# Optimization experiments

Measured on AMD Instinct MI355X. Metric: run time of the kernel, lower is better.

The kernel has to match this reference:

```python
import jax, jax.numpy as jnp
import numpy as np

B, L, D = 2, 2048, 4096
H, HKV = 32, 8
HD = D // H  # 128


def apply_rope(xq, xk, cos, sin):
    # xq: [B,L,H,HD], xk: [B,L,HKV,HD]; cos/sin: [L, HD//2]
    def rot(t):
        t2 = t.reshape(*t.shape[:-1], -1, 2)  # [..., HD//2, 2]
        tr, ti = t2[..., 0], t2[..., 1]
        c = cos[None, :, None, :]
        s = sin[None, :, None, :]
        out_r = tr * c - ti * s
        out_i = tr * s + ti * c
        return jnp.stack([out_r, out_i], axis=-1).reshape(t.shape)
    return rot(xq), rot(xk)


def setup_inputs() -> dict:
    key = jax.random.key(0)
    ks = jax.random.split(key, 5)
    sc = 0.02
    x = jax.random.normal(ks[0], (B, L, D), jnp.float32)
    wq = jax.random.normal(ks[1], (D, D), jnp.float32) * sc
    wk = jax.random.normal(ks[2], (HKV * HD, D), jnp.float32) * sc
    wv = jax.random.normal(ks[3], (HKV * HD, D), jnp.float32) * sc
    wo = jax.random.normal(ks[4], (D, D), jnp.float32) * sc
    # Llama RoPE tables
    inv_freq = 1.0 / (10000.0 ** (jnp.arange(0, HD, 2, dtype=jnp.float32) / HD))
    t = jnp.arange(L, dtype=jnp.float32)
    freqs = jnp.outer(t, inv_freq)  # [L, HD//2]
    cos, sin = jnp.cos(freqs), jnp.sin(freqs)
    # causal additive mask
    neg = jnp.float32(-1e9)
    mask = jnp.where(jnp.tril(jnp.ones((L, L), bool)), 0.0, neg)[None, None]
    return {"x": x, "wq": wq, "wk": wk, "wv": wv, "wo": wo,
            "cos": cos, "sin": sin, "mask": mask}


def reference(x, wq, wk, wv, wo, cos, sin, mask):
    Bx, Lx = x.shape[:2]
    xq = (x @ wq.T).reshape(Bx, Lx, H, HD)
    xk = (x @ wk.T).reshape(Bx, Lx, HKV, HD)
    xv = (x @ wv.T).reshape(Bx, Lx, HKV, HD)
    xq, xk = apply_rope(xq, xk, cos, sin)
    times = H // HKV
    xk = jnp.repeat(xk, times, axis=2)  # [B,L,H,HD]
    xv = jnp.repeat(xv, times, axis=2)
    # [B,H,L,L]
    scores = jnp.einsum('blhd,bmhd->bhlm', xq, xk) / jnp.sqrt(jnp.float32(HD))
    scores = scores + mask
    probs = jax.nn.softmax(scores.astype(jnp.float32), axis=-1).astype(xq.dtype)
    out = jnp.einsum('bhlm,bmhd->blhd', probs, xv).reshape(Bx, Lx, -1)
    return out @ wo.T
```

## Files before the change

kernel.cpp:

```cpp
#include <hip/hip_runtime.h>

#define BB 2
#define LL 2048
#define DD 4096
#define HH 32
#define NKV 8
#define HDIM 128
#define MROWS (BB*LL)

typedef __attribute__((ext_vector_type(8))) short bf16x8;
typedef __attribute__((ext_vector_type(8))) unsigned short u16x8;
typedef __attribute__((ext_vector_type(4))) unsigned short u16x4;
typedef __attribute__((ext_vector_type(4))) float f32x4;

#define MFMA16(a, b, c) __builtin_amdgcn_mfma_f32_16x16x32_bf16(a, b, c, 0, 0, 0)

__device__ __forceinline__ unsigned short f2bf(float x) {
  union { float f; unsigned u; } v; v.f = x;
  unsigned r = v.u + 0x7FFF + ((v.u >> 16) & 1);
  return (unsigned short)(r >> 16);
}
__device__ __forceinline__ float bf2f(unsigned short h) {
  union { unsigned u; float f; } v; v.u = ((unsigned)h) << 16; return v.f;
}
__device__ __forceinline__ unsigned packbf2(float lo, float hi) {
  return ((unsigned)f2bf(hi) << 16) | (unsigned)f2bf(lo);
}
__device__ __forceinline__ void gload_lds16(const void* g, void* l) {
  __builtin_amdgcn_global_load_lds(
      (const __attribute__((address_space(1))) unsigned int*)g,
      (__attribute__((address_space(3))) unsigned int*)l, 16, 0, 0);
}

__global__ __launch_bounds__(256) void cast_f32_bf16(
    const float* __restrict__ in, unsigned short* __restrict__ out, int n) {
  int stride = gridDim.x * blockDim.x * 4;
  for (int i = (blockIdx.x * blockDim.x + threadIdx.x) * 4; i < n; i += stride) {
    float4 v = *(const float4*)&in[i];
    u16x4 u;
    u[0] = f2bf(v.x); u[1] = f2bf(v.y); u[2] = f2bf(v.z); u[3] = f2bf(v.w);
    *(u16x4*)&out[i] = u;
  }
}

template <bool OUTBF>
__global__ __launch_bounds__(256) void gemm_bt(
    const unsigned short* __restrict__ A, const float* __restrict__ B,
    void* __restrict__ Cv, int M, int N, int K) {
  __shared__ unsigned short As[128 * 64];
  __shared__ unsigned short Bs[128 * 64];
  const int tid = threadIdx.x;
  const int lane = tid & 63, w = tid >> 6;
  const int l15 = lane & 15, lg = lane >> 4;
  const int wr = w >> 1, wc = w & 1;
  const int brow = blockIdx.y * 128, bcol = blockIdx.x * 128;

  f32x4 acc[4][4];
#pragma unroll
  for (int m = 0; m < 4; ++m)
#pragma unroll
    for (int n = 0; n < 4; ++n)
#pragma unroll
      for (int j = 0; j < 4; ++j) acc[m][n][j] = 0.f;

  for (int k0 = 0; k0 < K; k0 += 64) {
#pragma unroll
    for (int i = 0; i < 4; ++i) {
      int idx = i * 256 + tid;
      int row = idx >> 3, s = idx & 7;
      gload_lds16(&A[(size_t)(brow + row) * K + k0 + ((s ^ (row & 7)) * 8)],
                  &As[idx * 8]);
    }
#pragma unroll
    for (int i = 0; i < 4; ++i) {
      int f = i * 256 + tid;
      int row = f >> 3, s = f & 7;
      const float* src = &B[(size_t)(bcol + row) * K + k0 + ((s ^ (row & 7)) * 8)];
      float4 f0 = *(const float4*)src;
      float4 f1 = *(const float4*)(src + 4);
      u16x8 u;
      u[0] = f2bf(f0.x); u[1] = f2bf(f0.y); u[2] = f2bf(f0.z); u[3] = f2bf(f0.w);
      u[4] = f2bf(f1.x); u[5] = f2bf(f1.y); u[6] = f2bf(f1.z); u[7] = f2bf(f1.w);
      *(u16x8*)&Bs[f * 8] = u;
    }
    __syncthreads();
#pragma unroll
    for (int kk = 0; kk < 2; ++kk) {
      bf16x8 af[4], bfr[4];
      const int phys = (kk * 4 + lg) ^ (l15 & 7);
#pragma unroll
      for (int m = 0; m < 4; ++m) {
        int row = wr * 64 + m * 16 + l15;
        af[m] = *(const bf16x8*)&As[row * 64 + phys * 8];
      }
#pragma unroll
      for (int n = 0; n < 4; ++n) {
        int row = wc * 64 + n * 16 + l15;
        bfr[n] = *(const bf16x8*)&Bs[row * 64 + phys * 8];
      }
#pragma unroll
      for (int m = 0; m < 4; ++m)
#pragma unroll
        for (int n = 0; n < 4; ++n)
          acc[m][n] = MFMA16(af[m], bfr[n], acc[m][n]);
    }
    __syncthreads();
  }

#pragma unroll
  for (int m = 0; m < 4; ++m)
#pragma unroll
    for (int n = 0; n < 4; ++n)
#pragma unroll
      for (int j = 0; j < 4; ++j) {
        int r = brow + wr * 64 + m * 16 + lg * 4 + j;
        int c = bcol + wc * 64 + n * 16 + l15;
        if (OUTBF)
          ((unsigned short*)Cv)[(size_t)r * N + c] = f2bf(acc[m][n][j]);
        else
          ((float*)Cv)[(size_t)r * N + c] = acc[m][n][j];
      }
}

__global__ __launch_bounds__(256) void rope_bf16(
    unsigned* __restrict__ q, unsigned* __restrict__ k,
    const float* __restrict__ cosp, const float* __restrict__ sinp) {
  const int NQ = MROWS * (DD / 2);
  const int NT = NQ + MROWS * (NKV * HDIM / 2);
  int stride = gridDim.x * blockDim.x;
  for (int p = blockIdx.x * blockDim.x + threadIdx.x; p < NT; p += stride) {
    bool isq = p < NQ;
    int pp = isq ? p : p - NQ;
    int row = isq ? (pp >> 11) : (pp >> 9);
    int hp  = isq ? (pp & 2047) : (pp & 511);
    int i = hp & 63, l = row & (LL - 1);
    float c = cosp[l * 64 + i], s = sinp[l * 64 + i];
    unsigned* ptr = isq ? (q + (size_t)row * 2048 + hp)
                        : (k + (size_t)row * 512 + hp);
    unsigned v = *ptr;
    float tr = bf2f((unsigned short)(v & 0xffff));
    float ti = bf2f((unsigned short)(v >> 16));
    *ptr = packbf2(tr * c - ti * s, tr * s + ti * c);
  }
}

__global__ __launch_bounds__(256) void attn_mfma(
    const unsigned short* __restrict__ Qb, const unsigned short* __restrict__ Kb,
    const unsigned short* __restrict__ Vb, unsigned short* __restrict__ Ob) {
  __shared__ unsigned short Ks[64 * 128];
  __shared__ unsigned short Vt[128 * 64];
  const int tid = threadIdx.x;
  const int lane = tid & 63, w = tid >> 6;
  const int l15 = lane & 15, lg = lane >> 4;
  const int qt = (int)gridDim.x - 1 - (int)blockIdx.x;
  const int bh = blockIdx.y;
  const int b = bh >> 5, h = bh & 31, kvh = h >> 2;
  const int qrel = w * 16 + l15;
  const size_t qrow = (size_t)(b * LL + qt * 64 + qrel);

  bf16x8 qf[4];
#pragma unroll
  for (int c = 0; c < 4; ++c)
    qf[c] = *(const bf16x8*)&Qb[qrow * DD + h * HDIM + c * 32 + lg * 8];

  f32x4 oacc[8];
#pragma unroll
  for (int d = 0; d < 8; ++d)
#pragma unroll
    for (int j = 0; j < 4; ++j) oacc[d][j] = 0.f;
  float mrun = -1e30f, lrun = 0.f;
  const float scale = 0.08838834764831845f;

  for (int t0 = 0; t0 <= qt; ++t0) {
    const int k0 = t0 * 64;
#pragma unroll
    for (int i = 0; i < 4; ++i) {
      int idx = i * 256 + tid;
      int krow = idx >> 4, slot = idx & 15;
      gload_lds16(&Kb[(size_t)(b * LL + k0 + krow) * (NKV * HDIM) + kvh * HDIM +
                      ((slot ^ (krow & 15)) * 8)],
                  &Ks[idx * 8]);
    }
#pragma unroll
    for (int i = 0; i < 4; ++i) {
      int f = i * 256 + tid;
      int key = f & 63, d0 = (f >> 6) * 8;
      u16x8 v = *(const u16x8*)&Vb[(size_t)(b * LL + k0 + key) * (NKV * HDIM) +
                                   kvh * HDIM + d0];
#pragma unroll
      for (int j = 0; j < 8; ++j) {
        int dim = d0 + j;
        Vt[dim * 64 + (((key >> 3) ^ (dim & 7)) * 8) + (key & 7)] = v[j];
      }
    }
    __syncthreads();

    f32x4 sa[4];
#pragma unroll
    for (int mb = 0; mb < 4; ++mb) {
#pragma unroll
      for (int j = 0; j < 4; ++j) sa[mb][j] = 0.f;
#pragma unroll
      for (int c = 0; c < 4; ++c) {
        int row = mb * 16 + l15;
        int phys = (c * 4 + lg) ^ l15;
        bf16x8 kf = *(const bf16x8*)&Ks[row * 128 + phys * 8];
        sa[mb] = MFMA16(kf, qf[c], sa[mb]);
      }
    }

    const bool boundary = (t0 == qt);
#pragma unroll
    for (int mb = 0; mb < 4; ++mb)
#pragma unroll
      for (int j = 0; j < 4; ++j) {
        float s = sa[mb][j] * scale;
        if (boundary && (mb * 16 + lg * 4 + j > qrel)) s = -1e30f;
        sa[mb][j] = s;
      }
    float vm = -1e30f;
#pragma unroll
    for (int mb = 0; mb < 4; ++mb)
#pragma unroll
      for (int j = 0; j < 4; ++j) vm = fmaxf(vm, sa[mb][j]);
    vm = fmaxf(vm, __shfl_xor(vm, 16));
    vm = fmaxf(vm, __shfl_xor(vm, 32));
    float mnew = fmaxf(mrun, vm);
    float corr = __expf(mrun - mnew);
    float psum = 0.f;
#pragma unroll
    for (int mb = 0; mb < 4; ++mb)
#pragma unroll
      for (int j = 0; j < 4; ++j) {
        float p = __expf(sa[mb][j] - mnew);
        sa[mb][j] = p;
        psum += p;
      }
    psum += __shfl_xor(psum, 16);
    psum += __shfl_xor(psum, 32);
    lrun = lrun * corr + psum;
    mrun = mnew;
#pragma unroll
    for (int d = 0; d < 8; ++d)
#pragma unroll
      for (int j = 0; j < 4; ++j) oacc[d][j] *= corr;

    unsigned pk[4][2];
#pragma unroll
    for (int mb = 0; mb < 4; ++mb) {
      pk[mb][0] = packbf2(sa[mb][0], sa[mb][1]);
      pk[mb][1] = packbf2(sa[mb][2], sa[mb][3]);
    }

#pragma unroll
    for (int kh = 0; kh < 2; ++kh) {
      unsigned pbu[4];
#pragma unroll
      for (int r = 0; r < 4; ++r) {
        int srcl = l15 + 16 * ((lg & 1) * 2 + (r >> 1));
        unsigned va = (unsigned)__shfl((int)pk[2 * kh][r & 1], srcl);
        unsigned vb = (unsigned)__shfl((int)pk[2 * kh + 1][r & 1], srcl);
        pbu[r] = (lane & 32) ? vb : va;
      }
      bf16x8 pb;
#pragma unroll
      for (int r = 0; r < 4; ++r) {
        pb[2 * r]     = (short)(pbu[r] & 0xffff);
        pb[2 * r + 1] = (short)(pbu[r] >> 16);
      }
      const int phys = ((kh * 4 + lg) ^ (l15 & 7));
#pragma unroll
      for (int mbd = 0; mbd < 8; ++mbd) {
        int row = mbd * 16 + l15;
        bf16x8 vf = *(const bf16x8*)&Vt[row * 64 + phys * 8];
        oacc[mbd] = MFMA16(vf, pb, oacc[mbd]);
      }
    }
    __syncthreads();
  }

  float inv = 1.f / lrun;
#pragma unroll
  for (int mbd = 0; mbd < 8; ++mbd)
#pragma unroll
    for (int j = 0; j < 4; j += 2) {
      int dim = mbd * 16 + lg * 4 + j;
      unsigned pk2 = packbf2(oacc[mbd][j] * inv, oacc[mbd][j + 1] * inv);
      *(unsigned*)&Ob[qrow * DD + h * HDIM + dim] = pk2;
    }
}

extern "C" void kernel_launch(void* const* d_in, const int* in_sizes, int n_in,
                              void* d_out, int out_size, void* d_ws, size_t ws_size,
                              hipStream_t stream) {
  const float* x    = (const float*)d_in[0];
  const float* wq   = (const float*)d_in[1];
  const float* wk   = (const float*)d_in[2];
  const float* wv   = (const float*)d_in[3];
  const float* wo   = (const float*)d_in[4];
  const float* cosp = (const float*)d_in[5];
  const float* sinp = (const float*)d_in[6];
  float* out = (float*)d_out;

  unsigned short* xb     = (unsigned short*)d_ws;
  unsigned short* qbf    = xb + (size_t)MROWS * DD;
  unsigned short* kbf    = qbf + (size_t)MROWS * DD;
  unsigned short* vbf    = kbf + (size_t)MROWS * (NKV * HDIM);
  unsigned short* attnbf = vbf + (size_t)MROWS * (NKV * HDIM);

  dim3 blk(256);
  cast_f32_bf16<<<4096, blk, 0, stream>>>(x, xb, MROWS * DD);
  gemm_bt<true><<<dim3(DD / 128, MROWS / 128), blk, 0, stream>>>(
      xb, wq, qbf, MROWS, DD, DD);
  gemm_bt<true><<<dim3((NKV * HDIM) / 128, MROWS / 128), blk, 0, stream>>>(
      xb, wk, kbf, MROWS, NKV * HDIM, DD);
  gemm_bt<true><<<dim3((NKV * HDIM) / 128, MROWS / 128), blk, 0, stream>>>(
      xb, wv, vbf, MROWS, NKV * HDIM, DD);
  rope_bf16<<<8192, blk, 0, stream>>>((unsigned*)qbf, (unsigned*)kbf, cosp, sinp);
  attn_mfma<<<dim3(LL / 64, BB * HH), blk, 0, stream>>>(qbf, kbf, vbf, attnbf);
  gemm_bt<false><<<dim3(DD / 128, MROWS / 128), blk, 0, stream>>>(
      attnbf, wo, out, MROWS, DD, DD);
}
```

Baseline: 1.525 ms.

## Double-buffer K/V tiles in attention and prefetch next tile during compute

The attention kernel now keeps two LDS buffers for K and transposed V. The next K tile is issued as an async global-to-LDS load and the next V tile is loaded into registers before computing on the current tile, then written to the other buffer. This cuts the loop to one barrier per tile instead of two and hides global-load latency behind the MFMA and softmax work. It also raises MFMA wave priority with s_setprio. In exchange it doubles LDS use (to 64KB), which may lower occupancy, and holding V in registers adds register pressure.

```diff
diff --git a/kernel.cpp b/kernel.cpp
--- a/kernel.cpp
+++ b/kernel.cpp
@@ -147,8 +147,8 @@
 __global__ __launch_bounds__(256) void attn_mfma(
     const unsigned short* __restrict__ Qb, const unsigned short* __restrict__ Kb,
     const unsigned short* __restrict__ Vb, unsigned short* __restrict__ Ob) {
-  __shared__ unsigned short Ks[64 * 128];
-  __shared__ unsigned short Vt[128 * 64];
+  __shared__ unsigned short Ks[2][64 * 128];
+  __shared__ unsigned short Vt[2][128 * 64];
   const int tid = threadIdx.x;
   const int lane = tid & 63, w = tid >> 6;
   const int l15 = lane & 15, lg = lane >> 4;
@@ -171,31 +171,41 @@
   float mrun = -1e30f, lrun = 0.f;
   const float scale = 0.08838834764831845f;
 
-  for (int t0 = 0; t0 <= qt; ++t0) {
-    const int k0 = t0 * 64;
+  auto stageK = [&](int nb, int t) {
 #pragma unroll
     for (int i = 0; i < 4; ++i) {
       int idx = i * 256 + tid;
       int krow = idx >> 4, slot = idx & 15;
-      gload_lds16(&Kb[(size_t)(b * LL + k0 + krow) * (NKV * HDIM) + kvh * HDIM +
-                      ((slot ^ (krow & 15)) * 8)],
-                  &Ks[idx * 8]);
-    }
+      gload_lds16(&Kb[(size_t)(b * LL + t * 64 + krow) * (NKV * HDIM) +
+                      kvh * HDIM + ((slot ^ (krow & 15)) * 8)],
+                  &Ks[nb][idx * 8]);
+    }
+  };
+  auto loadV = [&](int t, u16x8* vreg) {
 #pragma unroll
     for (int i = 0; i < 4; ++i) {
       int f = i * 256 + tid;
       int key = f & 63, d0 = (f >> 6) * 8;
-      u16x8 v = *(const u16x8*)&Vb[(size_t)(b * LL + k0 + key) * (NKV * HDIM) +
-                                   kvh * HDIM + d0];
+      vreg[i] = *(const u16x8*)&Vb[(size_t)(b * LL + t * 64 + key) *
+                                   (NKV * HDIM) + kvh * HDIM + d0];
+    }
+  };
+  auto writeV = [&](int nb, const u16x8* vreg) {
+#pragma unroll
+    for (int i = 0; i < 4; ++i) {
+      int f = i * 256 + tid;
+      int key = f & 63, d0 = (f >> 6) * 8;
 #pragma unroll
       for (int j = 0; j < 8; ++j) {
         int dim = d0 + j;
-        Vt[dim * 64 + (((key >> 3) ^ (dim & 7)) * 8) + (key & 7)] = v[j];
-      }
-    }
-    __syncthreads();
-
+        Vt[nb][dim * 64 + (((key >> 3) ^ (dim & 7)) * 8) + (key & 7)] = vreg[i][j];
+      }
+    }
+  };
+
+  auto compute = [&](int nb, bool boundary) {
     f32x4 sa[4];
+    __builtin_amdgcn_s_setprio(1);
 #pragma unroll
     for (int mb = 0; mb < 4; ++mb) {
 #pragma unroll
@@ -204,12 +214,12 @@
       for (int c = 0; c < 4; ++c) {
         int row = mb * 16 + l15;
         int phys = (c * 4 + lg) ^ l15;
-        bf16x8 kf = *(const bf16x8*)&Ks[row * 128 + phys * 8];
+        bf16x8 kf = *(const bf16x8*)&Ks[nb][row * 128 + phys * 8];
         sa[mb] = MFMA16(kf, qf[c], sa[mb]);
       }
     }
-
-    const bool boundary = (t0 == qt);
+    __builtin_amdgcn_s_setprio(0);
+
 #pragma unroll
     for (int mb = 0; mb < 4; ++mb)
 #pragma unroll
@@ -269,15 +279,33 @@
         pb[2 * r + 1] = (short)(pbu[r] >> 16);
       }
       const int phys = ((kh * 4 + lg) ^ (l15 & 7));
+      __builtin_amdgcn_s_setprio(1);
 #pragma unroll
       for (int mbd = 0; mbd < 8; ++mbd) {
         int row = mbd * 16 + l15;
-        bf16x8 vf = *(const bf16x8*)&Vt[row * 64 + phys * 8];
+        bf16x8 vf = *(const bf16x8*)&Vt[nb][row * 64 + phys * 8];
         oacc[mbd] = MFMA16(vf, pb, oacc[mbd]);
       }
-    }
+      __builtin_amdgcn_s_setprio(0);
+    }
+  };
+
+  u16x8 vreg[4];
+  stageK(0, 0);
+  loadV(0, vreg);
+  writeV(0, vreg);
+  __syncthreads();
+
+  int cur = 0;
+  for (int t0 = 0; t0 < qt; ++t0) {
+    stageK(cur ^ 1, t0 + 1);
+    loadV(t0 + 1, vreg);
+    compute(cur, false);
+    writeV(cur ^ 1, vreg);
     __syncthreads();
+    cur ^= 1;
   }
+  compute(cur, true);
 
   float inv = 1.f / lrun;
 #pragma unroll
```

Result: faster. 1.230 ms (-19.4%).
